# Kernel optimization log

Measured on AMD Instinct MI355X. Metric: run time of the kernel, lower is better.

Reference implementation:

```python
import jax, jax.numpy as jnp
import numpy as np

B, H, W, C = 8, 56, 56, 256
HEADS = 8      # block-level heads; each branch uses HEADS//2
SPLIT = 7      # split_size
EPS = 1e-5


def _ln(x, g, b):
    m = x.mean(-1, keepdims=True)
    v = ((x - m) ** 2).mean(-1, keepdims=True)
    return (x - m) * jax.lax.rsqrt(v + EPS) * g + b


def _lepe_attn(q, k, v, H_sp, W_sp, heads, cw, cb):
    # q,k,v: [B,H,W,Ch]; cross-shaped window attention with LePE depthwise conv bias
    Bq, Hq, Wq, Ch = q.shape
    hd = Ch // heads
    scale = hd ** -0.5
    nh, nw = Hq // H_sp, Wq // W_sp

    def win(t):  # -> [Bw, heads, L, hd]  (Bw = B*nh*nw, L = H_sp*W_sp)
        t = t.reshape(Bq, nh, H_sp, nw, W_sp, Ch).transpose(0, 1, 3, 2, 4, 5)
        return t.reshape(-1, H_sp * W_sp, heads, hd).transpose(0, 2, 1, 3)

    qw, kw = win(q), win(k)
    # v windows laid out NCHW for the depthwise LePE conv
    vimg = v.reshape(Bq, nh, H_sp, nw, W_sp, Ch).transpose(0, 1, 3, 5, 2, 4).reshape(-1, Ch, H_sp, W_sp)
    lepe = jax.lax.conv_general_dilated(
        vimg, cw, window_strides=(1, 1), padding=((1, 1), (1, 1)),
        feature_group_count=Ch, dimension_numbers=("NCHW", "OIHW", "NCHW"))
    lepe = lepe + cb[None, :, None, None]
    lepe = lepe.reshape(-1, heads, hd, H_sp * W_sp).transpose(0, 1, 3, 2)
    vw = vimg.reshape(-1, heads, hd, H_sp * W_sp).transpose(0, 1, 3, 2)

    attn = jax.nn.softmax(jnp.einsum("whld,whmd->whlm", qw * scale, kw), axis=-1)
    out = jnp.einsum("whlm,whmd->whld", attn, vw) + lepe  # [Bw,heads,L,hd]
    out = out.transpose(0, 2, 1, 3).reshape(-1, H_sp, W_sp, Ch)
    # windows2img
    out = out.reshape(Bq, nh, nw, H_sp, W_sp, Ch).transpose(0, 1, 3, 2, 4, 5).reshape(Bq, Hq, Wq, Ch)
    return out


def setup_inputs() -> dict:
    key = jax.random.key(0)
    ks = jax.random.split(key, 8)
    ch = C // 2
    s = 0.02
    return {
        "x": jax.random.normal(ks[0], (B, H, W, C), jnp.float32),
        "gamma1": jnp.ones((C,), jnp.float32), "beta1": jnp.zeros((C,), jnp.float32),
        "w_qkv": jax.random.normal(ks[1], (C, 3 * C), jnp.float32) * s,
        "lepe_w0": jax.random.normal(ks[2], (ch, 1, 3, 3), jnp.float32) * s,
        "lepe_b0": jnp.zeros((ch,), jnp.float32),
        "lepe_w1": jax.random.normal(ks[3], (ch, 1, 3, 3), jnp.float32) * s,
        "lepe_b1": jnp.zeros((ch,), jnp.float32),
        "w_proj": jax.random.normal(ks[4], (C, C), jnp.float32) * s,
        "b_proj": jnp.zeros((C,), jnp.float32),
        "gamma2": jnp.ones((C,), jnp.float32), "beta2": jnp.zeros((C,), jnp.float32),
        "w_fc1": jax.random.normal(ks[5], (C, 4 * C), jnp.float32) * s,
        "b_fc1": jnp.zeros((4 * C,), jnp.float32),
        "w_fc2": jax.random.normal(ks[6], (4 * C, C), jnp.float32) * s,
        "b_fc2": jnp.zeros((C,), jnp.float32),
    }


def reference(x, gamma1, beta1, w_qkv, lepe_w0, lepe_b0, lepe_w1, lepe_b1,
              w_proj, b_proj, gamma2, beta2, w_fc1, b_fc1, w_fc2, b_fc2):
    Bx, Hx, Wx, Cx = x.shape
    img = _ln(x, gamma1, beta1)
    qkv = (img @ w_qkv).reshape(Bx, Hx, Wx, 3, Cx).transpose(3, 0, 1, 2, 4)
    q, k, v = qkv[0], qkv[1], qkv[2]
    ch = Cx // 2
    heads = HEADS // 2
    # branch 0 (idx=0): H_sp=H, W_sp=split  -> vertical stripes
    x0 = _lepe_attn(q[..., :ch], k[..., :ch], v[..., :ch], Hx, SPLIT, heads, lepe_w0, lepe_b0)
    # branch 1 (idx=1): H_sp=split, W_sp=W  -> horizontal stripes
    x1 = _lepe_attn(q[..., ch:], k[..., ch:], v[..., ch:], SPLIT, Wx, heads, lepe_w1, lepe_b1)
    att = jnp.concatenate([x0, x1], axis=-1) @ w_proj + b_proj
    x = x + att
    h = _ln(x, gamma2, beta2)
    h = jax.nn.gelu(h @ w_fc1 + b_fc1, approximate=False) @ w_fc2 + b_fc2
    return x + h
```

## Files before the change

### kernel.cpp

```cpp
#include <hip/hip_runtime.h>
#include <stdint.h>

typedef __attribute__((ext_vector_type(4))) float  f32x4;
typedef __attribute__((ext_vector_type(8))) __bf16 bf16x8;
typedef __attribute__((address_space(3))) uint16_t lds_u16;

#define DEVI static __device__ __forceinline__

DEVI float bf2f_lo(uint32_t u) { union { uint32_t i; float f; } v; v.i = u << 16;          return v.f; }
DEVI float bf2f_hi(uint32_t u) { union { uint32_t i; float f; } v; v.i = u & 0xffff0000u;  return v.f; }
DEVI uint16_t f2bf(float f) {
    union { float f; uint32_t i; } v; v.f = f;
    uint32_t r = v.i + 0x7fffu + ((v.i >> 16) & 1u);
    return (uint16_t)(r >> 16);
}
DEVI void unpack8(uint4 u, float* f) {
    f[0] = bf2f_lo(u.x); f[1] = bf2f_hi(u.x);
    f[2] = bf2f_lo(u.y); f[3] = bf2f_hi(u.y);
    f[4] = bf2f_lo(u.z); f[5] = bf2f_hi(u.z);
    f[6] = bf2f_lo(u.w); f[7] = bf2f_hi(u.w);
}
DEVI void gload_lds16(const uint16_t* gp, uint16_t* lp) {
    __builtin_amdgcn_global_load_lds(
        (const __attribute__((address_space(1))) uint32_t*)gp,
        (__attribute__((address_space(3))) uint32_t*)lp, 16, 0, 0);
}
DEVI uint2 trr(const lds_u16* a) {
    uint2 d;
    asm volatile("ds_read_b64_tr_b16 %0, %1" : "=v"(d) : "v"(a) : "memory");
    return d;
}

__global__ __launch_bounds__(256) void wprep4(const float* __restrict__ w_qkv,
                                              const float* __restrict__ w_proj,
                                              const float* __restrict__ w_fc1,
                                              const float* __restrict__ w_fc2,
                                              uint16_t* __restrict__ dqkv,
                                              uint16_t* __restrict__ dproj,
                                              uint16_t* __restrict__ dfc1,
                                              uint16_t* __restrict__ dfc2) {
    int idx = blockIdx.x * 256 + threadIdx.x;
    const float* w; uint16_t* d; int K, N;
    if (idx < 196608)      { w = w_qkv;  d = dqkv;  K = 256;  N = 768;  }
    else if (idx < 262144) { w = w_proj; d = dproj; K = 256;  N = 256;  idx -= 196608; }
    else if (idx < 524288) { w = w_fc1;  d = dfc1;  K = 256;  N = 1024; idx -= 262144; }
    else                   { w = w_fc2;  d = dfc2;  K = 1024; N = 256;  idx -= 524288; }
    int k = idx / N, n = idx - k * N;
    d[(size_t)n * K + k] = f2bf(w[idx]);
}

__global__ __launch_bounds__(256) void ln_kernel(const float* __restrict__ x,
                                                 const float* __restrict__ g,
                                                 const float* __restrict__ be,
                                                 uint16_t* __restrict__ y) {
    int row  = blockIdx.x * 4 + (threadIdx.x >> 6);
    int lane = threadIdx.x & 63;
    const float* xr = x + (size_t)row * 256 + lane * 4;
    f32x4 v = *(const f32x4*)xr;
    float s  = v[0] + v[1] + v[2] + v[3];
    float s2 = v[0]*v[0] + v[1]*v[1] + v[2]*v[2] + v[3]*v[3];
#pragma unroll
    for (int off = 32; off > 0; off >>= 1) {
        s  += __shfl_xor(s, off);
        s2 += __shfl_xor(s2, off);
    }
    float mean = s * (1.f / 256.f);
    float var  = s2 * (1.f / 256.f) - mean * mean;
    float rs   = rsqrtf(var + 1e-5f);
    f32x4 gv = *(const f32x4*)(g  + lane * 4);
    f32x4 bv = *(const f32x4*)(be + lane * 4);
    uint64_t pk = 0;
#pragma unroll
    for (int j = 0; j < 4; ++j) {
        uint64_t b = f2bf((v[j] - mean) * rs * gv[j] + bv[j]);
        pk |= b << (16 * j);
    }
    *(uint64_t*)(y + (size_t)row * 256 + lane * 4) = pk;
}

template <int EPI>
__global__ __launch_bounds__(256) void gemm_bt(const uint16_t* __restrict__ A,
                                               const uint16_t* __restrict__ Bt,
                                               int M, int N, int K,
                                               const float* __restrict__ bias,
                                               const float* __restrict__ resid,
                                               void* __restrict__ outp) {
    __shared__ __align__(16) uint16_t As[2][128 * 32];
    __shared__ __align__(16) uint16_t Bs[2][128 * 32];
    const int tid  = threadIdx.x;
    const int lane = tid & 63;
    const int w    = tid >> 6;
    const int wr   = w >> 1, wc = w & 1;
    const int bm = blockIdx.x, bn = blockIdx.y;
    f32x4 acc[4][4] = {};
    const int nk = K >> 5;
    const int wb = w * 512;

    const int srow = tid >> 2;
    const int hwr  = (srow ^ (srow >> 2)) & 3;
    const size_t ao0 = (size_t)srow * K + (size_t)(((tid & 3) ^ hwr) * 8);
    const size_t ao1 = ao0 + (size_t)64 * K;

    const uint16_t* Abase = A  + (size_t)bm * 128 * K;
    const uint16_t* Bbase = Bt + (size_t)bn * 128 * K;

    auto stage = [&](int buf, int kk) {
        const uint16_t* Ab = Abase + kk * 32;
        const uint16_t* Bb = Bbase + kk * 32;
        gload_lds16(Ab + ao0, &As[buf][wb]);
        gload_lds16(Ab + ao1, &As[buf][wb + 2048]);
        gload_lds16(Bb + ao0, &Bs[buf][wb]);
        gload_lds16(Bb + ao1, &Bs[buf][wb + 2048]);
    };

    stage(0, 0);
    __syncthreads();
    int cur = 0;

    const int li = lane & 15;
    const int rA = wr * 64 + li;
    const int rB = wc * 64 + li;
    const int kx = ((lane >> 4) ^ ((li ^ (li >> 2)) & 3)) * 8;

    for (int kk = 0; kk < nk; ++kk) {
        if (kk + 1 < nk) stage(cur ^ 1, kk + 1);

        bf16x8 af[4], bfr[4];
#pragma unroll
        for (int m = 0; m < 4; ++m)
            af[m] = __builtin_bit_cast(bf16x8,
                     *(const uint4*)&As[cur][(rA + m * 16) * 32 + kx]);
#pragma unroll
        for (int n = 0; n < 4; ++n)
            bfr[n] = __builtin_bit_cast(bf16x8,
                      *(const uint4*)&Bs[cur][(rB + n * 16) * 32 + kx]);
#pragma unroll
        for (int m = 0; m < 4; ++m)
#pragma unroll
            for (int n = 0; n < 4; ++n)
                acc[m][n] = __builtin_amdgcn_mfma_f32_16x16x32_bf16(af[m], bfr[n], acc[m][n], 0, 0, 0);

        __syncthreads();
        cur ^= 1;
    }

    const int row0 = bm * 128 + wr * 64 + ((lane >> 4) * 4);
    const int col0 = bn * 128 + wc * 64 + li;
#pragma unroll
    for (int m = 0; m < 4; ++m) {
#pragma unroll
        for (int n = 0; n < 4; ++n) {
            const int col = col0 + n * 16;
#pragma unroll
            for (int r = 0; r < 4; ++r) {
                const int row = row0 + m * 16 + r;
                float v = acc[m][n][r];
                size_t idx = (size_t)row * N + col;
                if (EPI == 0) {
                    ((uint16_t*)outp)[idx] = f2bf(v);
                } else if (EPI == 1) {
                    ((float*)outp)[idx] = v + bias[col] + resid[idx];
                } else {
                    v += bias[col];
                    float ge = 0.5f * v * (1.0f + erff(v * 0.70710678118654752f));
                    ((uint16_t*)outp)[idx] = f2bf(ge);
                }
            }
        }
    }
}

__global__ __launch_bounds__(64) void attn_mfma(const uint16_t* __restrict__ qkv,
                                                uint16_t* __restrict__ att) {
    __shared__ __align__(16) uint16_t Pl[32 * 40];
    __shared__ __align__(16) uint16_t Vb[2][2][32][16];
    int bid = ((int)blockIdx.x & 7) * 832 + ((int)blockIdx.x >> 3);
    const int sub   = bid % 52;
    const int winl  = bid / 52;
    const int qtile = sub % 13;
    const int head  = sub / 13;
    const int win   = winl & 63;
    const int branch = winl >> 6;
    const int lane = threadIdx.x;
    const int g  = lane >> 4;
    const int li = lane & 15;
    const int b = win >> 3, wp = win & 7;
    const int ch0 = branch * 128 + head * 32;
    const int base0 = b * 3136;
    const int woff  = wp * 7;
    const int toks1 = base0 + wp * 392;

    auto tokof = [&](int l) -> int {
        if (branch == 0) { int r = l / 7; return base0 + r * 56 + woff + (l - r * 7); }
        return toks1 + l;
    };
    auto vtok = [&](int key) -> int { return tokof(key > 391 ? 391 : key); };
    const int q0 = qtile * 32;

    const int skey = lane >> 1;
    const int sch  = (lane & 1) * 8;

    bf16x8 qf[2];
#pragma unroll
    for (int nb = 0; nb < 2; ++nb) {
        int ql = q0 + nb * 16 + li; if (ql > 391) ql = 391;
        qf[nb] = __builtin_bit_cast(bf16x8,
                 *(const uint4*)(qkv + (size_t)tokof(ql) * 768 + ch0 + g * 8));
    }

    float s_run[2] = {0.f, 0.f};
    f32x4 oacc[2][2];
#pragma unroll
    for (int nb = 0; nb < 2; ++nb) { oacc[0][nb] = (f32x4)0.f; oacc[1][nb] = (f32x4)0.f; }
    const float c = 0.25503486f;

    {
        const uint16_t* vp = qkv + (size_t)vtok(skey) * 768 + 512 + ch0 + sch;
        uint4 ra = *(const uint4*)vp;
        uint4 rb = *(const uint4*)(vp + 16);
        *(uint4*)&Vb[0][0][skey][sch] = ra;
        *(uint4*)&Vb[0][1][skey][sch] = rb;
    }
    int cur = 0;

    for (int kt = 0; kt < 13; ++kt) {
        const int kbase = kt * 32;
        bf16x8 kf[2];
#pragma unroll
        for (int mb = 0; mb < 2; ++mb) {
            int kl = kbase + mb * 16 + li; if (kl > 391) kl = 391;
            kf[mb] = __builtin_bit_cast(bf16x8,
                     *(const uint4*)(qkv + (size_t)tokof(kl) * 768 + 256 + ch0 + g * 8));
        }
        uint4 ra, rb;
        const bool more = (kt + 1 < 13);
        if (more) {
            const uint16_t* vp = qkv + (size_t)vtok(kbase + 32 + skey) * 768 + 512 + ch0 + sch;
            ra = *(const uint4*)vp;
            rb = *(const uint4*)(vp + 16);
        }
        f32x4 sa[2][2] = {};
#pragma unroll
        for (int mb = 0; mb < 2; ++mb)
#pragma unroll
            for (int nb = 0; nb < 2; ++nb)
                sa[mb][nb] = __builtin_amdgcn_mfma_f32_16x16x32_bf16(kf[mb], qf[nb], sa[mb][nb], 0, 0, 0);
        if (kt == 12) {
#pragma unroll
            for (int nb = 0; nb < 2; ++nb)
#pragma unroll
                for (int r = 0; r < 4; ++r) {
                    if (g >= 2) sa[0][nb][r] = -1e30f;
                    sa[1][nb][r] = -1e30f;
                }
        }
#pragma unroll
        for (int nb = 0; nb < 2; ++nb) {
            float psum = 0.f;
            uint32_t pk[4];
#pragma unroll
            for (int mb = 0; mb < 2; ++mb) {
                float p0 = exp2f(sa[mb][nb][0] * c);
                float p1 = exp2f(sa[mb][nb][1] * c);
                float p2 = exp2f(sa[mb][nb][2] * c);
                float p3 = exp2f(sa[mb][nb][3] * c);
                psum += (p0 + p1) + (p2 + p3);
                union { __bf16 h[2]; uint32_t u; } ca, cb;
                ca.h[0] = (__bf16)p0; ca.h[1] = (__bf16)p1;
                cb.h[0] = (__bf16)p2; cb.h[1] = (__bf16)p3;
                pk[mb * 2 + 0] = ca.u;
                pk[mb * 2 + 1] = cb.u;
            }
            psum += __shfl_xor(psum, 16);
            psum += __shfl_xor(psum, 32);
            s_run[nb] += psum;
            uint32_t* dst = (uint32_t*)&Pl[(li + 16 * nb) * 40];
            dst[g * 2 + 0] = pk[0];
            dst[g * 2 + 1] = pk[1];
            dst[g * 2 + 8] = pk[2];
            dst[g * 2 + 9] = pk[3];
        }
        if (more) {
            *(uint4*)&Vb[cur ^ 1][0][skey][sch] = ra;
            *(uint4*)&Vb[cur ^ 1][1][skey][sch] = rb;
        }
        const lds_u16* vb = (const lds_u16*)&Vb[cur][0][0][0];
        const lds_u16* p0 = vb + g * 128 + li;
        uint2 t0 = trr(p0);
        uint2 t1 = trr(p0 + 64);
        uint2 t2 = trr(p0 + 512);
        uint2 t3 = trr(p0 + 512 + 64);
        asm volatile("s_waitcnt lgkmcnt(0)" ::: "memory");
        __builtin_amdgcn_sched_barrier(0);
        bf16x8 vf0 = __builtin_bit_cast(bf16x8, uint4{t0.x, t0.y, t1.x, t1.y});
        bf16x8 vf1 = __builtin_bit_cast(bf16x8, uint4{t2.x, t2.y, t3.x, t3.y});

        bf16x8 pf[2];
#pragma unroll
        for (int nb = 0; nb < 2; ++nb)
            pf[nb] = __builtin_bit_cast(bf16x8,
                     *(const uint4*)&Pl[(li + 16 * nb) * 40 + g * 8]);
#pragma unroll
        for (int nb = 0; nb < 2; ++nb) {
            oacc[0][nb] = __builtin_amdgcn_mfma_f32_16x16x32_bf16(vf0, pf[nb], oacc[0][nb], 0, 0, 0);
            oacc[1][nb] = __builtin_amdgcn_mfma_f32_16x16x32_bf16(vf1, pf[nb], oacc[1][nb], 0, 0, 0);
        }
        cur ^= 1;
    }
#pragma unroll
    for (int nb = 0; nb < 2; ++nb) {
        int ql = q0 + nb * 16 + li;
        if (ql <= 391) {
            float rn = 1.f / s_run[nb];
            uint16_t* op = att + (size_t)tokof(ql) * 256 + ch0;
#pragma unroll
            for (int mb = 0; mb < 2; ++mb)
#pragma unroll
                for (int r = 0; r < 4; ++r)
                    op[mb * 16 + g * 4 + r] = f2bf(oacc[mb][nb][r] * rn);
        }
    }
}

__global__ __launch_bounds__(256) void lepe_kernel(const uint16_t* __restrict__ qkv,
                                                   const float* __restrict__ lw0,
                                                   const float* __restrict__ lb0,
                                                   const float* __restrict__ lw1,
                                                   const float* __restrict__ lb1,
                                                   uint16_t* __restrict__ att) {
    __shared__ float wl[9][256];
    __shared__ float bl[256];
    {
        int tid = threadIdx.x;
        for (int i = tid; i < 2304; i += 256) {
            int tap = i >> 8, ch = i & 255;
            wl[tap][ch] = (ch < 128) ? lw0[ch * 9 + tap] : lw1[(ch - 128) * 9 + tap];
        }
        bl[tid] = (tid < 128) ? lb0[tid] : lb1[tid - 128];
    }
    __syncthreads();

    int idx = blockIdx.x * 256 + threadIdx.x;
    int t = idx >> 5, cg = idx & 31;
    int ch = cg * 8;
    int branch = ch >> 7;
    int b = t / 3136, rem = t - b * 3136, h = rem / 56, w = rem - h * 56;
    int r0, r1, c0, c1;
    if (branch == 0) { r0 = 0; r1 = 55; int wp = w / 7; c0 = wp * 7; c1 = c0 + 6; }
    else             { int hp = h / 7; r0 = hp * 7; r1 = r0 + 6; c0 = 0; c1 = 55; }

    const uint16_t* vbase = qkv + (size_t)b * 3136 * 768 + 512 + ch;
    float acc[8];
    {
        f32x4 b0 = *(const f32x4*)&bl[ch];
        f32x4 b1 = *(const f32x4*)&bl[ch + 4];
#pragma unroll
        for (int d = 0; d < 4; ++d) { acc[d] = b0[d]; acc[d + 4] = b1[d]; }
    }
#pragma unroll
    for (int dy = -1; dy <= 1; ++dy) {
#pragma unroll
        for (int dx = -1; dx <= 1; ++dx) {
            int hh = h + dy, ww = w + dx;
            float mask = (hh >= r0 && hh <= r1 && ww >= c0 && ww <= c1) ? 1.f : 0.f;
            int hc = min(max(hh, r0), r1), wc = min(max(ww, c0), c1);
            uint4 u = *(const uint4*)(vbase + (size_t)(hc * 56 + wc) * 768);
            float vv[8]; unpack8(u, vv);
            const int tap = (dy + 1) * 3 + (dx + 1);
            f32x4 w0 = *(const f32x4*)&wl[tap][ch];
            f32x4 w1 = *(const f32x4*)&wl[tap][ch + 4];
#pragma unroll
            for (int d = 0; d < 4; ++d) {
                acc[d]     += (mask * w0[d]) * vv[d];
                acc[d + 4] += (mask * w1[d]) * vv[d + 4];
            }
        }
    }
    uint16_t* ap = att + (size_t)t * 256 + ch;
    uint4 a = *(const uint4*)ap;
    float av[8]; unpack8(a, av);
    uint16_t ob[8];
#pragma unroll
    for (int d = 0; d < 8; ++d) ob[d] = f2bf(av[d] + acc[d]);
    *(uint4*)ap = *(const uint4*)ob;
}

extern "C" void kernel_launch(void* const* d_in, const int* in_sizes, int n_in,
                              void* d_out, int out_size, void* d_ws, size_t ws_size,
                              hipStream_t stream) {
    const float* x      = (const float*)d_in[0];
    const float* g1     = (const float*)d_in[1];
    const float* be1    = (const float*)d_in[2];
    const float* w_qkv  = (const float*)d_in[3];
    const float* lw0    = (const float*)d_in[4];
    const float* lb0    = (const float*)d_in[5];
    const float* lw1    = (const float*)d_in[6];
    const float* lb1    = (const float*)d_in[7];
    const float* w_proj = (const float*)d_in[8];
    const float* b_proj = (const float*)d_in[9];
    const float* g2     = (const float*)d_in[10];
    const float* be2    = (const float*)d_in[11];
    const float* w_fc1  = (const float*)d_in[12];
    const float* b_fc1  = (const float*)d_in[13];
    const float* w_fc2  = (const float*)d_in[14];
    const float* b_fc2  = (const float*)d_in[15];
    float* out = (float*)d_out;

    char* p = (char*)d_ws;
    auto carve = [&](size_t bytes) -> char* {
        char* q = p; p += (bytes + 255) & ~(size_t)255; return q;
    };
    uint16_t* lnb    = (uint16_t*)carve((size_t)25088 * 256 * 2);
    uint16_t* qkvh   = (uint16_t*)carve((size_t)25088 * 1024 * 2);
    uint16_t* attb   = (uint16_t*)carve((size_t)25088 * 256 * 2);
    float*    x1     = (float*)   carve((size_t)25088 * 256 * 4);
    uint16_t* wqkvT  = (uint16_t*)carve((size_t)768 * 256 * 2);
    uint16_t* wprojT = (uint16_t*)carve((size_t)256 * 256 * 2);
    uint16_t* wfc1T  = (uint16_t*)carve((size_t)1024 * 256 * 2);
    uint16_t* wfc2T  = (uint16_t*)carve((size_t)256 * 1024 * 2);

    wprep4<<<3072, 256, 0, stream>>>(w_qkv, w_proj, w_fc1, w_fc2,
                                     wqkvT, wprojT, wfc1T, wfc2T);

    ln_kernel<<<6272, 256, 0, stream>>>(x, g1, be1, lnb);
    gemm_bt<0><<<dim3(196, 6), 256, 0, stream>>>(lnb, wqkvT, 25088, 768, 256,
                                                 nullptr, nullptr, qkvh);
    attn_mfma<<<6656, 64, 0, stream>>>(qkvh, attb);
    lepe_kernel<<<3136, 256, 0, stream>>>(qkvh, lw0, lb0, lw1, lb1, attb);
    gemm_bt<1><<<dim3(196, 2), 256, 0, stream>>>(attb, wprojT, 25088, 256, 256,
                                                 b_proj, x, x1);
    ln_kernel<<<6272, 256, 0, stream>>>(x1, g2, be2, lnb);
    gemm_bt<2><<<dim3(196, 8), 256, 0, stream>>>(lnb, wfc1T, 25088, 1024, 256,
                                                 b_fc1, nullptr, qkvh);
    gemm_bt<1><<<dim3(196, 2), 256, 0, stream>>>(qkvh, wfc2T, 25088, 256, 1024,
                                                 b_fc2, x1, out);
}
```

Measured before the change: 281.3 us.

## Restructure GEMMs to stage full-K weight tiles in LDS and stream A from global

Replaces the double-buffered 128x128x32 LDS GEMM with a kernel that loads a 64-column x 256-K slice of the weight matrix into swizzled LDS per chunk and reads A fragments directly from global memory into registers. Tiles shrink to 128x64, which doubles the grid along N and removes per-k-step barriers and A staging. In exchange, A is re-read from global/L2 once per N tile with uncoalesced 16-byte row loads. There is also no overlap between the B loads and compute within a chunk.

```diff
diff --git a/kernel.cpp b/kernel.cpp
--- a/kernel.cpp
+++ b/kernel.cpp
@@ -78,83 +78,71 @@
     *(uint64_t*)(y + (size_t)row * 256 + lane * 4) = pk;
 }
 
-template <int EPI>
-__global__ __launch_bounds__(256) void gemm_bt(const uint16_t* __restrict__ A,
+template <int EPI, int NKC>
+__global__ __launch_bounds__(256) void gemm_ws(const uint16_t* __restrict__ A,
                                                const uint16_t* __restrict__ Bt,
                                                int M, int N, int K,
                                                const float* __restrict__ bias,
                                                const float* __restrict__ resid,
                                                void* __restrict__ outp) {
-    __shared__ __align__(16) uint16_t As[2][128 * 32];
-    __shared__ __align__(16) uint16_t Bs[2][128 * 32];
+    __shared__ __align__(16) uint16_t Bs[64 * 256];
     const int tid  = threadIdx.x;
     const int lane = tid & 63;
     const int w    = tid >> 6;
-    const int wr   = w >> 1, wc = w & 1;
+    const int wm   = w >> 1, wn = w & 1;
+    const int g    = lane >> 4;
+    const int li   = lane & 15;
     const int bm = blockIdx.x, bn = blockIdx.y;
-    f32x4 acc[4][4] = {};
-    const int nk = K >> 5;
-    const int wb = w * 512;
-
-    const int srow = tid >> 2;
-    const int hwr  = (srow ^ (srow >> 2)) & 3;
-    const size_t ao0 = (size_t)srow * K + (size_t)(((tid & 3) ^ hwr) * 8);
-    const size_t ao1 = ao0 + (size_t)64 * K;
-
-    const uint16_t* Abase = A  + (size_t)bm * 128 * K;
-    const uint16_t* Bbase = Bt + (size_t)bn * 128 * K;
-
-    auto stage = [&](int buf, int kk) {
-        const uint16_t* Ab = Abase + kk * 32;
-        const uint16_t* Bb = Bbase + kk * 32;
-        gload_lds16(Ab + ao0, &As[buf][wb]);
-        gload_lds16(Ab + ao1, &As[buf][wb + 2048]);
-        gload_lds16(Bb + ao0, &Bs[buf][wb]);
-        gload_lds16(Bb + ao1, &Bs[buf][wb + 2048]);
-    };
-
-    stage(0, 0);
-    __syncthreads();
-    int cur = 0;
-
-    const int li = lane & 15;
-    const int rA = wr * 64 + li;
-    const int rB = wc * 64 + li;
-    const int kx = ((lane >> 4) ^ ((li ^ (li >> 2)) & 3)) * 8;
-
-    for (int kk = 0; kk < nk; ++kk) {
-        if (kk + 1 < nk) stage(cur ^ 1, kk + 1);
-
-        bf16x8 af[4], bfr[4];
-#pragma unroll
-        for (int m = 0; m < 4; ++m)
-            af[m] = __builtin_bit_cast(bf16x8,
-                     *(const uint4*)&As[cur][(rA + m * 16) * 32 + kx]);
-#pragma unroll
-        for (int n = 0; n < 4; ++n)
-            bfr[n] = __builtin_bit_cast(bf16x8,
-                      *(const uint4*)&Bs[cur][(rB + n * 16) * 32 + kx]);
-#pragma unroll
-        for (int m = 0; m < 4; ++m)
-#pragma unroll
-            for (int n = 0; n < 4; ++n)
-                acc[m][n] = __builtin_amdgcn_mfma_f32_16x16x32_bf16(af[m], bfr[n], acc[m][n], 0, 0, 0);
-
+
+    f32x4 acc[4][2] = {};
+    const uint16_t* Arow = A + (size_t)(bm * 128 + wm * 64 + li) * K;
+    const int swz = li & 7;
+
+    for (int kc = 0; kc < NKC; ++kc) {
         __syncthreads();
-        cur ^= 1;
-    }
-
-    const int row0 = bm * 128 + wr * 64 + ((lane >> 4) * 4);
-    const int col0 = bn * 128 + wc * 64 + li;
-#pragma unroll
-    for (int m = 0; m < 4; ++m) {
-#pragma unroll
-        for (int n = 0; n < 4; ++n) {
-            const int col = col0 + n * 16;
+#pragma unroll
+        for (int i = 0; i < 8; ++i) {
+            int c = i * 256 + tid;
+            int row = c >> 5, ccol = c & 31;
+            const uint16_t* src = Bt + (size_t)(bn * 64 + row) * K + kc * 256
+                                     + ((ccol ^ (row & 7)) * 8);
+            gload_lds16(src, &Bs[(i * 256 + w * 64) * 8]);
+        }
+        __syncthreads();
+
+        const uint16_t* Ak = Arow + kc * 256;
+#pragma unroll
+        for (int kk = 0; kk < 8; ++kk) {
+            bf16x8 af[4], bf[2];
+#pragma unroll
+            for (int mb = 0; mb < 4; ++mb)
+                af[mb] = __builtin_bit_cast(bf16x8,
+                          *(const uint4*)(Ak + (size_t)mb * 16 * K + kk * 32 + g * 8));
+#pragma unroll
+            for (int nb = 0; nb < 2; ++nb) {
+                int nloc = wn * 32 + nb * 16 + li;
+                bf[nb] = __builtin_bit_cast(bf16x8,
+                          *(const uint4*)&Bs[nloc * 256 + (((kk * 4 + g) ^ swz) * 8)]);
+            }
+#pragma unroll
+            for (int mb = 0; mb < 4; ++mb)
+#pragma unroll
+                for (int nb = 0; nb < 2; ++nb)
+                    acc[mb][nb] = __builtin_amdgcn_mfma_f32_16x16x32_bf16(af[mb], bf[nb], acc[mb][nb], 0, 0, 0);
+        }
+    }
+
+    const int row0 = bm * 128 + wm * 64 + g * 4;
+    const int col0 = bn * 64 + wn * 32 + li;
+#pragma unroll
+    for (int mb = 0; mb < 4; ++mb) {
+#pragma unroll
+        for (int nb = 0; nb < 2; ++nb) {
+            const int col = col0 + nb * 16;
 #pragma unroll
             for (int r = 0; r < 4; ++r) {
-                const int row = row0 + m * 16 + r;
-                float v = acc[m][n][r];
+                const int row = row0 + mb * 16 + r;
+                float v = acc[mb][nb][r];
                 size_t idx = (size_t)row * N + col;
                 if (EPI == 0) {
                     ((uint16_t*)outp)[idx] = f2bf(v);
@@ -423,15 +411,15 @@
                                      wqkvT, wprojT, wfc1T, wfc2T);
 
     ln_kernel<<<6272, 256, 0, stream>>>(x, g1, be1, lnb);
-    gemm_bt<0><<<dim3(196, 6), 256, 0, stream>>>(lnb, wqkvT, 25088, 768, 256,
-                                                 nullptr, nullptr, qkvh);
+    gemm_ws<0, 1><<<dim3(196, 12), 256, 0, stream>>>(lnb, wqkvT, 25088, 768, 256,
+                                                     nullptr, nullptr, qkvh);
     attn_mfma<<<6656, 64, 0, stream>>>(qkvh, attb);
     lepe_kernel<<<3136, 256, 0, stream>>>(qkvh, lw0, lb0, lw1, lb1, attb);
-    gemm_bt<1><<<dim3(196, 2), 256, 0, stream>>>(attb, wprojT, 25088, 256, 256,
-                                                 b_proj, x, x1);
+    gemm_ws<1, 1><<<dim3(196, 4), 256, 0, stream>>>(attb, wprojT, 25088, 256, 256,
+                                                    b_proj, x, x1);
     ln_kernel<<<6272, 256, 0, stream>>>(x1, g2, be2, lnb);
-    gemm_bt<2><<<dim3(196, 8), 256, 0, stream>>>(lnb, wfc1T, 25088, 1024, 256,
-                                                 b_fc1, nullptr, qkvh);
-    gemm_bt<1><<<dim3(196, 2), 256, 0, stream>>>(qkvh, wfc2T, 25088, 256, 1024,
-                                                 b_fc2, x1, out);
-}
+    gemm_ws<2, 1><<<dim3(196, 16), 256, 0, stream>>>(lnb, wfc1T, 25088, 1024, 256,
+                                                     b_fc1, nullptr, qkvh);
+    gemm_ws<1, 4><<<dim3(196, 4), 256, 0, stream>>>(qkvh, wfc2T, 25088, 256, 1024,
+                                                    b_fc2, x1, out);
+}
```

After: 382.4 us. 35.9% more time.
